# Performance work log

Hardware: AMD Instinct MI355X
Metric: run time of the kernel (lower is better)

The kernel has to match this reference:

```python
import jax, jax.numpy as jnp
import numpy as np

NV, NE, NT = 20000, 40000, 30000
D, H, L = 512, 8, 2
HD = D // H
SCALE = float(np.sqrt(HD))
EV, EE, ET = 160000, 160000, 120000
LN_EPS = 1e-5


def _layer_norm(x, g, b):
    m = jnp.mean(x, axis=-1, keepdims=True)
    v = jnp.mean((x - m) ** 2, axis=-1, keepdims=True)
    return (x - m) * jax.lax.rsqrt(v + LN_EPS) * g + b


def _attn_layer(x, ei, W, b, g, bt):
    # x: [N, D]; ei: [2, E]; W: [4, D, D] (q,k,v,out); b: [4, D]
    n = x.shape[0]
    resid = x
    q = (x @ W[0] + b[0]).reshape(n, H, HD)
    k = (x @ W[1] + b[1]).reshape(n, H, HD)
    v = (x @ W[2] + b[2]).reshape(n, H, HD)
    src, dst = ei[0], ei[1]
    # per-edge scores: query at target, key at source (k[edge_index[1]] gather in original)
    scores = jnp.sum(q[dst] * k[src], axis=-1) / SCALE        # [E, H]
    # NOTE: original applies softmax over dim=0, i.e. globally over the edge axis
    w = jax.nn.softmax(scores, axis=0)                         # [E, H]
    msgs = w[:, :, None] * v[src]                              # [E, H, HD]
    out = jax.ops.segment_sum(msgs, dst, num_segments=n)      # [N, H, HD]
    out = out.reshape(n, D) @ W[3] + b[3]
    return _layer_norm(out + resid, g, bt)


def _attn_stack(x, ei, W, b, g, bt):
    for l in range(L):
        x = _attn_layer(x, ei, W[l], b[l], g[l], bt[l])
    return x


def setup_inputs() -> dict:
    key = jax.random.key(0)
    ks = jax.random.split(key, 16)
    inp = {}
    inp['vertices'] = jax.random.normal(ks[0], (NV, D), jnp.float32)
    inp['edge_features'] = jax.random.normal(ks[1], (NE, D), jnp.float32)
    inp['triangle_features'] = jax.random.normal(ks[2], (NT, D), jnp.float32)
    inp['v_embed'] = jax.random.normal(ks[3], (NV, D), jnp.float32)
    inp['e_embed'] = jax.random.normal(ks[4], (NE, D), jnp.float32)
    inp['t_embed'] = jax.random.normal(ks[5], (NT, D), jnp.float32)
    inp['v_pos'] = jax.random.normal(ks[6], (NV, D), jnp.float32) * 0.1
    inp['e_pos'] = jax.random.normal(ks[7], (NE, D), jnp.float32) * 0.1
    inp['t_pos'] = jax.random.normal(ks[8], (NT, D), jnp.float32) * 0.1
    for name, k2 in (('v', ks[9]), ('e', ks[10]), ('t', ks[11])):
        inp[name + 'W'] = jax.random.normal(k2, (L, 4, D, D), jnp.float32) * 0.02
        inp[name + 'B'] = jnp.zeros((L, 4, D), jnp.float32)
        inp[name + 'G'] = jnp.ones((L, D), jnp.float32)
        inp[name + 'Bt'] = jnp.zeros((L, D), jnp.float32)
    inp['head_W'] = jax.random.normal(ks[12], (3, D, D), jnp.float32) * 0.02
    inp['head_b'] = jnp.zeros((3, D), jnp.float32)
    inp['v_ei'] = jax.random.randint(ks[13], (2, EV), 0, NV, jnp.int32)
    inp['e_ei'] = jax.random.randint(ks[14], (2, EE), 0, NE, jnp.int32)
    inp['t_ei'] = jax.random.randint(ks[15], (2, ET), 0, NT, jnp.int32)
    return inp


def reference(vertices, edge_features, triangle_features, v_embed, e_embed, t_embed,
              v_pos, e_pos, t_pos, vW, vB, vG, vBt, eW, eB, eG, eBt,
              tW, tB, tG, tBt, head_W, head_b, v_ei, e_ei, t_ei):
    # embedding(arange(N)) == full table lookup; add positional params and input features
    v = v_embed + v_pos + vertices
    e = e_embed + e_pos + edge_features
    t = t_embed + t_pos + triangle_features
    v = _attn_stack(v, v_ei, vW, vB, vG, vBt)
    e = _attn_stack(e, e_ei, eW, eB, eG, eBt)
    t = _attn_stack(t, t_ei, tW, tB, tG, tBt)
    v_out = v @ head_W[0] + head_b[0]
    e_out = e @ head_W[1] + head_b[1]
    t_out = t @ head_W[2] + head_b[2]
    return (v_out, e_out, t_out)
```

## Files before the change

### kernel.cpp

```cpp
#include <hip/hip_runtime.h>


typedef __attribute__((ext_vector_type(8))) __bf16 bf16x8;
typedef __attribute__((ext_vector_type(4))) float f32x4;
typedef __attribute__((ext_vector_type(8))) unsigned short ushort8v;
typedef __attribute__((ext_vector_type(4))) unsigned short ushort4v;

__device__ __forceinline__ float b2f(unsigned short u) {
  union { unsigned u; float f; } x; x.u = (unsigned)u << 16; return x.f;
}
__device__ __forceinline__ unsigned short f2b(float f) {
  union { float f; unsigned u; } x; x.f = f;
  unsigned r = x.u + 0x7fffu + ((x.u >> 16) & 1u);
  return (unsigned short)(r >> 16);
}

__global__ __launch_bounds__(256) void init_x_kernel(
    const float4* __restrict__ a, const float4* __restrict__ b,
    const float4* __restrict__ c, float4* __restrict__ x,
    unsigned short* __restrict__ xb, long long n4)
{
  long long stride = (long long)gridDim.x * 256;
  for (long long i = (long long)blockIdx.x * 256 + threadIdx.x; i < n4; i += stride) {
    float4 av = a[i], bv = b[i], cv = c[i];
    float4 r;
    r.x = av.x + bv.x + cv.x; r.y = av.y + bv.y + cv.y;
    r.z = av.z + bv.z + cv.z; r.w = av.w + bv.w + cv.w;
    x[i] = r;
    ushort4v o; o.x = f2b(r.x); o.y = f2b(r.y); o.z = f2b(r.z); o.w = f2b(r.w);
    *(ushort4v*)(xb + i * 4) = o;
  }
}

__global__ __launch_bounds__(256) void transpose_w_kernel(
    const float* __restrict__ W, unsigned short* __restrict__ WT)
{
  __shared__ float t[32][33];
  const float* src = W + (size_t)blockIdx.z * 262144;
  unsigned short* dst = WT + (size_t)blockIdx.z * 262144;
  int bx = blockIdx.x * 32, by = blockIdx.y * 32;
  int tx = threadIdx.x, ty = threadIdx.y;
  #pragma unroll
  for (int i = 0; i < 32; i += 8)
    t[ty + i][tx] = src[(size_t)(by + ty + i) * 512 + bx + tx];
  __syncthreads();
  #pragma unroll
  for (int i = 0; i < 32; i += 8) {
    int c = bx + ty + i;
    int p = (c & ~0x3C) | ((c & 0x30) >> 2) | ((c & 0x0C) << 2);
    dst[(size_t)p * 512 + by + tx] = f2b(t[tx][ty + i]);
  }
}

__device__ __forceinline__ void stage16(const void* g, void* lds_uniform) {
  __builtin_amdgcn_global_load_lds(
      (const __attribute__((address_space(1))) void*)g,
      (__attribute__((address_space(3))) void*)lds_uniform, 16, 0, 0);
}

template<int OUT_BF16>
__global__ __launch_bounds__(256) void gemm_bt_kernel(
    const unsigned short* __restrict__ A,
    const unsigned short* __restrict__ BT,
    const float* __restrict__ bias,
    void* __restrict__ Cv,
    int M, int Ncols)
{
  constexpr int K = 512;
  __shared__ unsigned short smem[32768];

  const int nwg = gridDim.x, orig = blockIdx.x;
  const int xcd = orig & 7, lin = orig >> 3;
  const int q = nwg >> 3, r8 = nwg & 7;
  const int wgid = (xcd < r8 ? xcd * (q + 1) : r8 * (q + 1) + (xcd - r8) * q) + lin;

  const int tiles_n = Ncols >> 7;
  const int tm = wgid / tiles_n;
  const int tn = wgid - tm * tiles_n;
  const int row0 = tm << 7, col0 = tn << 7;
  const int lane = threadIdx.x & 63, wid = threadIdx.x >> 6;
  const int wm = (wid >> 1) << 6, wn = (wid & 1) << 6;

  f32x4 acc[4][4];
  #pragma unroll
  for (int i = 0; i < 4; ++i)
    #pragma unroll
    for (int j = 0; j < 4; ++j) acc[i][j] = (f32x4)0.f;

  int srow[4], scsw[4], sseg[4];
  #pragma unroll
  for (int i = 0; i < 4; ++i) {
    int seg = (i << 2) | wid;
    int idx = (seg << 6) | lane;
    int row = idx >> 3, ch = idx & 7;
    sseg[i] = seg; srow[i] = row; scsw[i] = ch ^ (row & 7);
  }

  #define STAGE(buf, kb_)                                                      \
    _Pragma("unroll")                                                          \
    for (int i = 0; i < 4; ++i) {                                              \
      int ra = row0 + srow[i]; ra = (ra < M) ? ra : (M - 1);                   \
      stage16(A + (size_t)ra * K + (kb_) + (scsw[i] << 3),                     \
              smem + (buf) * 16384 + (sseg[i] << 9));                          \
      int rb = col0 + srow[i];                                                 \
      stage16(BT + (size_t)rb * K + (kb_) + (scsw[i] << 3),                    \
              smem + (buf) * 16384 + 8192 + (sseg[i] << 9));                   \
    }

  STAGE(0, 0)
  asm volatile("s_waitcnt vmcnt(0)" ::: "memory");
  __syncthreads();

  #pragma unroll
  for (int kt = 0; kt < 8; ++kt) {
    const int cur = kt & 1;
    if (kt < 7) {
      STAGE(cur ^ 1, (kt + 1) << 6)
    }
    const unsigned short* As = smem + cur * 16384;
    const unsigned short* Bs = As + 8192;
    #pragma unroll
    for (int kk = 0; kk < 2; ++kk) {
      const int kb = (kk << 6) + ((lane >> 4) << 4);
      bf16x8 af[4], bfr[4];
      #pragma unroll
      for (int mi = 0; mi < 4; ++mi) {
        int r = wm + (mi << 4) + (lane & 15);
        af[mi] = *(const bf16x8*)((const char*)As + (r << 7) + (kb ^ ((r & 7) << 4)));
      }
      #pragma unroll
      for (int ni = 0; ni < 4; ++ni) {
        int r = wn + (ni << 4) + (lane & 15);
        bfr[ni] = *(const bf16x8*)((const char*)Bs + (r << 7) + (kb ^ ((r & 7) << 4)));
      }
      #pragma unroll
      for (int mi = 0; mi < 4; ++mi)
        #pragma unroll
        for (int ni = 0; ni < 4; ++ni)
          acc[mi][ni] = __builtin_amdgcn_mfma_f32_16x16x32_bf16(
              bfr[ni], af[mi], acc[mi][ni], 0, 0, 0);
    }
    asm volatile("s_waitcnt vmcnt(0)" ::: "memory");
    __syncthreads();
  }
  #undef STAGE

  const int mrow = lane & 15;
  const int t4 = (lane >> 4) << 4;
  float bsv[16];
  #pragma unroll
  for (int ni = 0; ni < 4; ++ni) {
    float4 bv = *(const float4*)(bias + col0 + wn + t4 + (ni << 2));
    bsv[4*ni+0] = bv.x; bsv[4*ni+1] = bv.y; bsv[4*ni+2] = bv.z; bsv[4*ni+3] = bv.w;
  }

  if (OUT_BF16) {
    unsigned short* C = (unsigned short*)Cv;
    #pragma unroll
    for (int mi = 0; mi < 4; ++mi) {
      int rowg = row0 + wm + (mi << 4) + mrow;
      if (rowg < M) {
        ushort8v o0, o1;
        #pragma unroll
        for (int r = 0; r < 4; ++r) {
          o0[r]     = f2b(acc[mi][0][r] + bsv[r]);
          o0[4 + r] = f2b(acc[mi][1][r] + bsv[4 + r]);
          o1[r]     = f2b(acc[mi][2][r] + bsv[8 + r]);
          o1[4 + r] = f2b(acc[mi][3][r] + bsv[12 + r]);
        }
        unsigned short* cp = C + (size_t)rowg * Ncols + col0 + wn + t4;
        *(ushort8v*)cp = o0;
        *(ushort8v*)(cp + 8) = o1;
      }
    }
  } else {
    float* C = (float*)Cv;
    #pragma unroll
    for (int mi = 0; mi < 4; ++mi) {
      int rowg = row0 + wm + (mi << 4) + mrow;
      if (rowg < M) {
        float* cp = C + (size_t)rowg * Ncols + col0 + wn + t4;
        #pragma unroll
        for (int ni = 0; ni < 4; ++ni) {
          float4 v;
          v.x = acc[mi][ni][0] + bsv[4*ni+0];
          v.y = acc[mi][ni][1] + bsv[4*ni+1];
          v.z = acc[mi][ni][2] + bsv[4*ni+2];
          v.w = acc[mi][ni][3] + bsv[4*ni+3];
          *(float4*)(cp + (ni << 2)) = v;
        }
      }
    }
  }
}

__global__ __launch_bounds__(256) void csr_scores_kernel(
    const unsigned short* __restrict__ qkv, const int* __restrict__ srcs,
    const int* __restrict__ rowptr, int N, float* __restrict__ sc)
{
  int wid = threadIdx.x >> 6, lane = threadIdx.x & 63;
  int n = (blockIdx.x << 2) | wid;
  if (n >= N) return;
  int beg = rowptr[n], end = rowptr[n + 1];
  if (beg == end) return;
  ushort8v qv = *(const ushort8v*)(qkv + (size_t)n * 1536 + (lane << 3));
  float qf[8];
  #pragma unroll
  for (int j = 0; j < 8; ++j) qf[j] = b2f(qv[j]);
  int i = beg;
  for (; i + 2 <= end; i += 2) {
    int s0 = srcs[i], s1 = srcs[i + 1];
    ushort8v k0 = *(const ushort8v*)(qkv + (size_t)s0 * 1536 + 512 + (lane << 3));
    ushort8v k1 = *(const ushort8v*)(qkv + (size_t)s1 * 1536 + 512 + (lane << 3));
    float p0 = 0.f, p1 = 0.f;
    #pragma unroll
    for (int j = 0; j < 8; ++j) { p0 += qf[j] * b2f(k0[j]); p1 += qf[j] * b2f(k1[j]); }
    p0 += __shfl_xor(p0, 1); p1 += __shfl_xor(p1, 1);
    p0 += __shfl_xor(p0, 2); p1 += __shfl_xor(p1, 2);
    p0 += __shfl_xor(p0, 4); p1 += __shfl_xor(p1, 4);
    if (!(lane & 7)) {
      sc[(size_t)i * 8 + (lane >> 3)] = p0 * 0.125f;
      sc[(size_t)(i + 1) * 8 + (lane >> 3)] = p1 * 0.125f;
    }
  }
  if (i < end) {
    int s0 = srcs[i];
    ushort8v k0 = *(const ushort8v*)(qkv + (size_t)s0 * 1536 + 512 + (lane << 3));
    float p0 = 0.f;
    #pragma unroll
    for (int j = 0; j < 8; ++j) p0 += qf[j] * b2f(k0[j]);
    p0 += __shfl_xor(p0, 1);
    p0 += __shfl_xor(p0, 2);
    p0 += __shfl_xor(p0, 4);
    if (!(lane & 7)) sc[(size_t)i * 8 + (lane >> 3)] = p0 * 0.125f;
  }
}

template<int OP>
__device__ __forceinline__ void reduce8_block(float (&v)[8], float* red) {
  int lane = threadIdx.x & 63, wid = threadIdx.x >> 6;
  #pragma unroll
  for (int h = 0; h < 8; ++h)
    #pragma unroll
    for (int off = 1; off < 64; off <<= 1) {
      float o = __shfl_xor(v[h], off);
      v[h] = OP ? (v[h] + o) : fmaxf(v[h], o);
    }
  if (lane == 0) {
    #pragma unroll
    for (int h = 0; h < 8; ++h) red[h * 4 + wid] = v[h];
  }
  __syncthreads();
  if (threadIdx.x == 0) {
    #pragma unroll
    for (int h = 0; h < 8; ++h) {
      float r = red[h * 4];
      #pragma unroll
      for (int w = 1; w < 4; ++w)
        r = OP ? (r + red[h * 4 + w]) : fmaxf(r, red[h * 4 + w]);
      v[h] = r;
    }
  }
}

__global__ __launch_bounds__(256) void sm_max_partial_kernel(
    const float* __restrict__ sc, int E, float* __restrict__ part)
{
  __shared__ float red[32];
  float v[8];
  #pragma unroll
  for (int h = 0; h < 8; ++h) v[h] = -1e30f;
  int stride = gridDim.x * 256;
  for (int e = blockIdx.x * 256 + threadIdx.x; e < E; e += stride) {
    #pragma unroll
    for (int h = 0; h < 8; ++h) v[h] = fmaxf(v[h], sc[(size_t)e * 8 + h]);
  }
  reduce8_block<0>(v, red);
  if (threadIdx.x == 0) {
    #pragma unroll
    for (int h = 0; h < 8; ++h) part[blockIdx.x * 8 + h] = v[h];
  }
}

__global__ __launch_bounds__(256) void sm_exp_partial_kernel(
    float* __restrict__ sc, int E, const float* __restrict__ partm,
    float* __restrict__ parts)
{
  __shared__ float red[32];
  __shared__ float gmx[8];
  float v[8];
  #pragma unroll
  for (int h = 0; h < 8; ++h) v[h] = partm[threadIdx.x * 8 + h];
  reduce8_block<0>(v, red);
  if (threadIdx.x == 0) {
    #pragma unroll
    for (int h = 0; h < 8; ++h) gmx[h] = v[h];
  }
  __syncthreads();
  float gm[8];
  #pragma unroll
  for (int h = 0; h < 8; ++h) { gm[h] = gmx[h]; v[h] = 0.f; }
  int stride = gridDim.x * 256;
  for (int e = blockIdx.x * 256 + threadIdx.x; e < E; e += stride) {
    #pragma unroll
    for (int h = 0; h < 8; ++h) {
      float w = __expf(sc[(size_t)e * 8 + h] - gm[h]);
      sc[(size_t)e * 8 + h] = w;
      v[h] += w;
    }
  }
  reduce8_block<1>(v, red);
  if (threadIdx.x == 0) {
    #pragma unroll
    for (int h = 0; h < 8; ++h) parts[blockIdx.x * 8 + h] = v[h];
  }
}

template<int OP>
__global__ __launch_bounds__(256) void sm_final_kernel(
    const float* __restrict__ part, float* __restrict__ out)
{
  __shared__ float red[32];
  float v[8];
  #pragma unroll
  for (int h = 0; h < 8; ++h) v[h] = part[threadIdx.x * 8 + h];
  reduce8_block<OP>(v, red);
  if (threadIdx.x == 0) {
    #pragma unroll
    for (int h = 0; h < 8; ++h) out[h] = OP ? (1.0f / v[h]) : v[h];
  }
}

__global__ __launch_bounds__(256) void hist_kernel(
    const int* __restrict__ ei, int E, int* __restrict__ deg)
{
  int e = blockIdx.x * 256 + threadIdx.x;
  if (e < E) atomicAdd(&deg[ei[E + e]], 1);
}

__global__ __launch_bounds__(1024) void scan_part_kernel(
    const int* __restrict__ deg, int N, int* __restrict__ rowptr,
    int* __restrict__ bsums)
{
  __shared__ int wsum[16];
  int i = blockIdx.x * 1024 + threadIdx.x;
  int lane = threadIdx.x & 63, wid = threadIdx.x >> 6;
  int sv = (i < N) ? deg[i] : 0;
  #pragma unroll
  for (int off = 1; off < 64; off <<= 1) {
    int t = __shfl_up(sv, off);
    if (lane >= off) sv += t;
  }
  if (lane == 63) wsum[wid] = sv;
  __syncthreads();
  if (threadIdx.x < 16) {
    int ws = wsum[threadIdx.x];
    #pragma unroll
    for (int off = 1; off < 16; off <<= 1) {
      int t = __shfl_up(ws, off);
      if (threadIdx.x >= off) ws += t;
    }
    wsum[threadIdx.x] = ws;
  }
  __syncthreads();
  if (wid > 0) sv += wsum[wid - 1];
  if (i < N) rowptr[i + 1] = sv;
  if (threadIdx.x == 1023) bsums[blockIdx.x] = sv;
}

__global__ __launch_bounds__(64) void scan_bsums_kernel(int* bsums, int nb)
{
  int lane = threadIdx.x;
  int v = (lane < nb) ? bsums[lane] : 0;
  #pragma unroll
  for (int off = 1; off < 64; off <<= 1) {
    int t = __shfl_up(v, off);
    if (lane >= off) v += t;
  }
  int ex = __shfl_up(v, 1);
  if (lane == 0) ex = 0;
  if (lane < nb) bsums[lane] = ex;
}

__global__ __launch_bounds__(1024) void scan_add_kernel(
    int* __restrict__ rowptr, const int* __restrict__ bsums, int N)
{
  int i = blockIdx.x * 1024 + threadIdx.x;
  if (i == 0) rowptr[0] = 0;
  if (i < N && blockIdx.x > 0) rowptr[i + 1] += bsums[blockIdx.x];
}

__global__ __launch_bounds__(256) void scatter_kernel(
    const int* __restrict__ ei, int E, const int* __restrict__ rowptr,
    int* __restrict__ cur, int* __restrict__ srcs)
{
  int e = blockIdx.x * 256 + threadIdx.x;
  if (e < E) {
    int dst = ei[E + e];
    int pos = atomicAdd(&cur[dst], 1);
    srcs[rowptr[dst] + pos] = ei[e];
  }
}

__global__ __launch_bounds__(256) void aggregate_kernel(
    const unsigned short* __restrict__ qkv, const float* __restrict__ wexp,
    const float* __restrict__ ginv, const int* __restrict__ srcs,
    const int* __restrict__ rowptr, int N, unsigned short* __restrict__ agg)
{
  int wid = threadIdx.x >> 6, lane = threadIdx.x & 63;
  int n = (blockIdx.x << 2) | wid;
  if (n >= N) return;
  int beg = rowptr[n], end = rowptr[n + 1];
  int h = lane >> 3;
  float inv = ginv[h];
  float acc[8] = {0.f,0.f,0.f,0.f,0.f,0.f,0.f,0.f};
  int i = beg;
  for (; i + 2 <= end; i += 2) {
    int s0 = srcs[i], s1 = srcs[i + 1];
    float w0 = wexp[(size_t)i * 8 + h] * inv;
    float w1 = wexp[(size_t)(i + 1) * 8 + h] * inv;
    ushort8v v0 = *(const ushort8v*)(qkv + (size_t)s0 * 1536 + 1024 + (lane << 3));
    ushort8v v1 = *(const ushort8v*)(qkv + (size_t)s1 * 1536 + 1024 + (lane << 3));
    #pragma unroll
    for (int j = 0; j < 8; ++j) acc[j] += w0 * b2f(v0[j]) + w1 * b2f(v1[j]);
  }
  if (i < end) {
    int s0 = srcs[i];
    float w0 = wexp[(size_t)i * 8 + h] * inv;
    ushort8v v0 = *(const ushort8v*)(qkv + (size_t)s0 * 1536 + 1024 + (lane << 3));
    #pragma unroll
    for (int j = 0; j < 8; ++j) acc[j] += w0 * b2f(v0[j]);
  }
  ushort8v o;
  #pragma unroll
  for (int j = 0; j < 8; ++j) o[j] = f2b(acc[j]);
  *(ushort8v*)(agg + (size_t)n * 512 + (lane << 3)) = o;
}

__global__ __launch_bounds__(256) void ln_kernel(
    const unsigned short* __restrict__ proj, const float* __restrict__ g,
    const float* __restrict__ bt, float* __restrict__ x,
    unsigned short* __restrict__ xb, int N)
{
  int wid = threadIdx.x >> 6, lane = threadIdx.x & 63;
  int n = (blockIdx.x << 2) | wid;
  if (n >= N) return;
  size_t base = (size_t)n * 512 + (lane << 3);
  ushort8v pv = *(const ushort8v*)(proj + base);
  const float4* xp = (const float4*)(x + base);
  float4 x0 = xp[0], x1 = xp[1];
  float y[8] = {b2f(pv[0]) + x0.x, b2f(pv[1]) + x0.y, b2f(pv[2]) + x0.z,
                b2f(pv[3]) + x0.w, b2f(pv[4]) + x1.x, b2f(pv[5]) + x1.y,
                b2f(pv[6]) + x1.z, b2f(pv[7]) + x1.w};
  float s = 0.f;
  #pragma unroll
  for (int j = 0; j < 8; ++j) s += y[j];
  #pragma unroll
  for (int off = 1; off < 64; off <<= 1) s += __shfl_xor(s, off);
  float mean = s * (1.f / 512.f);
  float vs = 0.f;
  #pragma unroll
  for (int j = 0; j < 8; ++j) { float d = y[j] - mean; vs += d * d; }
  #pragma unroll
  for (int off = 1; off < 64; off <<= 1) vs += __shfl_xor(vs, off);
  float rstd = rsqrtf(vs * (1.f / 512.f) + 1e-5f);
  int gi = lane << 3;
  float o[8];
  #pragma unroll
  for (int j = 0; j < 8; ++j) o[j] = (y[j] - mean) * rstd * g[gi + j] + bt[gi + j];
  float4 r0 = {o[0], o[1], o[2], o[3]}, r1 = {o[4], o[5], o[6], o[7]};
  *(float4*)(x + base) = r0;
  *(float4*)(x + base + 4) = r1;
  ushort8v ob;
  #pragma unroll
  for (int j = 0; j < 8; ++j) ob[j] = f2b(o[j]);
  *(ushort8v*)(xb + base) = ob;
}

extern "C" void kernel_launch(void* const* d_in, const int* in_sizes, int n_in,
                              void* d_out, int out_size, void* d_ws, size_t ws_size,
                              hipStream_t stream)
{
  (void)n_in; (void)out_size;
  const float* feat[3] = {(const float*)d_in[0], (const float*)d_in[1], (const float*)d_in[2]};
  const float* emb[3]  = {(const float*)d_in[3], (const float*)d_in[4], (const float*)d_in[5]};
  const float* pos[3]  = {(const float*)d_in[6], (const float*)d_in[7], (const float*)d_in[8]};
  const float* W[3]  = {(const float*)d_in[9],  (const float*)d_in[13], (const float*)d_in[17]};
  const float* Bb[3] = {(const float*)d_in[10], (const float*)d_in[14], (const float*)d_in[18]};
  const float* G[3]  = {(const float*)d_in[11], (const float*)d_in[15], (const float*)d_in[19]};
  const float* Bt[3] = {(const float*)d_in[12], (const float*)d_in[16], (const float*)d_in[20]};
  const float* headW = (const float*)d_in[21];
  const float* headB = (const float*)d_in[22];
  const int* ei[3] = {(const int*)d_in[23], (const int*)d_in[24], (const int*)d_in[25]};

  int Ns[3], Es[3];
  for (int s = 0; s < 3; ++s) { Ns[s] = in_sizes[s] / 512; Es[s] = in_sizes[23 + s] / 2; }
  int NMAX = Ns[0], EMAX = Es[0];
  for (int s = 1; s < 3; ++s) { if (Ns[s] > NMAX) NMAX = Ns[s]; if (Es[s] > EMAX) EMAX = Es[s]; }

  char* base = (char*)d_ws;
  size_t off = 0;
  auto carve = [&](size_t bytes) -> char* {
    char* r = base + off;
    off += (bytes + 255) & ~(size_t)255;
    return r;
  };
  unsigned short* WT  = (unsigned short*)carve((size_t)27 * 262144 * 2);
  float*          X   = (float*)carve((size_t)NMAX * 512 * 4);
  unsigned short* XB  = (unsigned short*)carve((size_t)NMAX * 512 * 2);
  unsigned short* QKV = (unsigned short*)carve((size_t)NMAX * 1536 * 2);
  float*          SC  = (float*)carve((size_t)EMAX * 8 * 4);
  unsigned short* AGG = (unsigned short*)carve((size_t)NMAX * 512 * 2);
  int*   ROWPTR = (int*)carve((size_t)(NMAX + 1) * 4);
  int*   DEG    = (int*)carve((size_t)NMAX * 4);
  int*   SRCS   = (int*)carve((size_t)EMAX * 4);
  int*   BSUMS  = (int*)carve(64 * 4);
  float* PARTM  = (float*)carve(256 * 8 * 4);
  float* PARTS  = (float*)carve(256 * 8 * 4);
  float* GINV   = (float*)carve(256);
  unsigned short* PROJ = QKV;
  if (off > ws_size) return;

  transpose_w_kernel<<<dim3(16,16,8), dim3(32,8), 0, stream>>>(W[0], WT);
  transpose_w_kernel<<<dim3(16,16,8), dim3(32,8), 0, stream>>>(W[1], WT + (size_t)8 * 262144);
  transpose_w_kernel<<<dim3(16,16,8), dim3(32,8), 0, stream>>>(W[2], WT + (size_t)16 * 262144);
  transpose_w_kernel<<<dim3(16,16,3), dim3(32,8), 0, stream>>>(headW, WT + (size_t)24 * 262144);

  size_t out_off = 0;
  for (int s = 0; s < 3; ++s) {
    const int N = Ns[s], E = Es[s];
    const int mt = (N + 127) >> 7;
    const int nb = (N + 1023) / 1024;

    init_x_kernel<<<2048, 256, 0, stream>>>(
        (const float4*)feat[s], (const float4*)emb[s], (const float4*)pos[s],
        (float4*)X, XB, (long long)N * 128);

    hipMemsetAsync(DEG, 0, (size_t)N * 4, stream);
    hist_kernel<<<(E + 255) / 256, 256, 0, stream>>>(ei[s], E, DEG);
    scan_part_kernel<<<nb, 1024, 0, stream>>>(DEG, N, ROWPTR, BSUMS);
    scan_bsums_kernel<<<1, 64, 0, stream>>>(BSUMS, nb);
    scan_add_kernel<<<nb, 1024, 0, stream>>>(ROWPTR, BSUMS, N);
    hipMemsetAsync(DEG, 0, (size_t)N * 4, stream);
    scatter_kernel<<<(E + 255) / 256, 256, 0, stream>>>(ei[s], E, ROWPTR, DEG, SRCS);

    for (int l = 0; l < 2; ++l) {
      const unsigned short* Wqkv = WT + (size_t)(s * 8 + l * 4) * 262144;
      const unsigned short* Wo   = WT + (size_t)(s * 8 + l * 4 + 3) * 262144;
      const float* bqkv = Bb[s] + (size_t)l * 4 * 512;
      const float* bo   = Bb[s] + (size_t)(l * 4 + 3) * 512;

      gemm_bt_kernel<1><<<dim3(mt * 12), 256, 0, stream>>>(XB, Wqkv, bqkv, QKV, N, 1536);
      csr_scores_kernel<<<(N + 3) / 4, 256, 0, stream>>>(QKV, SRCS, ROWPTR, N, SC);
      sm_max_partial_kernel<<<256, 256, 0, stream>>>(SC, E, PARTM);
      sm_exp_partial_kernel<<<256, 256, 0, stream>>>(SC, E, PARTM, PARTS);
      sm_final_kernel<1><<<1, 256, 0, stream>>>(PARTS, GINV);
      aggregate_kernel<<<(N + 3) / 4, 256, 0, stream>>>(QKV, SC, GINV, SRCS, ROWPTR, N, AGG);
      gemm_bt_kernel<1><<<dim3(mt * 4), 256, 0, stream>>>(AGG, Wo, bo, PROJ, N, 512);
      ln_kernel<<<(N + 3) / 4, 256, 0, stream>>>(PROJ, G[s] + (size_t)l * 512,
                                                 Bt[s] + (size_t)l * 512, X, XB, N);
    }

    gemm_bt_kernel<0><<<dim3(mt * 4), 256, 0, stream>>>(
        XB, WT + (size_t)(24 + s) * 262144, headB + (size_t)s * 512,
        (float*)d_out + out_off, N, 512);
    out_off += (size_t)N * 512;
  }
}
```

Measured before the change: 1.498 ms.

## Retile bf16 GEMM to 256x256 blocks with 8 waves and interleaved staging

Enlarges the GEMM block tile from 128x128 to 256x256 and doubles the block to 512 threads, each wave holding an 8x4 accumulator tile. The next k-tile's async global-to-LDS loads are split into halves and interleaved with MFMA phases, separated by barriers and with wave priority raised around the MFMAs. The aim is more data reuse per LDS byte and better overlap of loads with compute. In exchange it uses 128KB of LDS, so only one block fits per CU, and the 512-column GEMMs launch far fewer blocks, which risks underfilling the GPU. It also drops the explicit vmcnt wait before consuming staged data.

Measured after the change: 1.496 ms. About the same (-0.1%).

```diff
diff --git a/kernel.cpp b/kernel.cpp
--- a/kernel.cpp
+++ b/kernel.cpp
@@ -59,7 +59,7 @@
 }
 
 template<int OUT_BF16>
-__global__ __launch_bounds__(256) void gemm_bt_kernel(
+__global__ __launch_bounds__(512, 2) void gemm_bt_kernel(
     const unsigned short* __restrict__ A,
     const unsigned short* __restrict__ BT,
     const float* __restrict__ bias,
@@ -67,98 +67,140 @@
     int M, int Ncols)
 {
   constexpr int K = 512;
-  __shared__ unsigned short smem[32768];
+  __shared__ unsigned short smem[65536];
 
   const int nwg = gridDim.x, orig = blockIdx.x;
   const int xcd = orig & 7, lin = orig >> 3;
   const int q = nwg >> 3, r8 = nwg & 7;
   const int wgid = (xcd < r8 ? xcd * (q + 1) : r8 * (q + 1) + (xcd - r8) * q) + lin;
 
-  const int tiles_n = Ncols >> 7;
+  const int tiles_n = Ncols >> 8;
   const int tm = wgid / tiles_n;
   const int tn = wgid - tm * tiles_n;
-  const int row0 = tm << 7, col0 = tn << 7;
+  const int row0 = tm << 8, col0 = tn << 8;
   const int lane = threadIdx.x & 63, wid = threadIdx.x >> 6;
-  const int wm = (wid >> 1) << 6, wn = (wid & 1) << 6;
-
-  f32x4 acc[4][4];
-  #pragma unroll
-  for (int i = 0; i < 4; ++i)
+  const int wr = (wid >> 2) << 7;
+  const int wc = (wid & 3) << 6;
+
+  f32x4 acc[8][4];
+  #pragma unroll
+  for (int i = 0; i < 8; ++i)
     #pragma unroll
     for (int j = 0; j < 4; ++j) acc[i][j] = (f32x4)0.f;
 
   int srow[4], scsw[4], sseg[4];
   #pragma unroll
   for (int i = 0; i < 4; ++i) {
-    int seg = (i << 2) | wid;
+    int seg = (i << 3) | wid;
     int idx = (seg << 6) | lane;
     int row = idx >> 3, ch = idx & 7;
     sseg[i] = seg; srow[i] = row; scsw[i] = ch ^ (row & 7);
   }
 
-  #define STAGE(buf, kb_)                                                      \
-    _Pragma("unroll")                                                          \
-    for (int i = 0; i < 4; ++i) {                                              \
-      int ra = row0 + srow[i]; ra = (ra < M) ? ra : (M - 1);                   \
-      stage16(A + (size_t)ra * K + (kb_) + (scsw[i] << 3),                     \
-              smem + (buf) * 16384 + (sseg[i] << 9));                          \
-      int rb = col0 + srow[i];                                                 \
-      stage16(BT + (size_t)rb * K + (kb_) + (scsw[i] << 3),                    \
-              smem + (buf) * 16384 + 8192 + (sseg[i] << 9));                   \
-    }
-
-  STAGE(0, 0)
-  asm volatile("s_waitcnt vmcnt(0)" ::: "memory");
+  #define STG_PAIR(buf, kb_, i)                                               \
+    { int ra = row0 + srow[i]; ra = (ra < M) ? ra : (M - 1);                  \
+      stage16(A + (size_t)ra * K + (kb_) + (scsw[i] << 3),                    \
+              smem + (buf) * 32768 + (sseg[i] << 9));                         \
+      int rb = col0 + srow[i];                                                \
+      stage16(BT + (size_t)rb * K + (kb_) + (scsw[i] << 3),                   \
+              smem + (buf) * 32768 + 16384 + (sseg[i] << 9)); }
+
+  STG_PAIR(0, 0, 0) STG_PAIR(0, 0, 1) STG_PAIR(0, 0, 2) STG_PAIR(0, 0, 3)
   __syncthreads();
 
+  const int lm = lane & 15;
+  const int kbl = (lane >> 4) << 4;
+
   #pragma unroll
   for (int kt = 0; kt < 8; ++kt) {
-    const int cur = kt & 1;
-    if (kt < 7) {
-      STAGE(cur ^ 1, (kt + 1) << 6)
-    }
-    const unsigned short* As = smem + cur * 16384;
-    const unsigned short* Bs = As + 8192;
-    #pragma unroll
-    for (int kk = 0; kk < 2; ++kk) {
-      const int kb = (kk << 6) + ((lane >> 4) << 4);
-      bf16x8 af[4], bfr[4];
+    const int cur = kt & 1, nxt = cur ^ 1, kb1 = (kt + 1) << 6;
+    const char* Asb = (const char*)(smem + cur * 32768);
+    const char* Bsb = Asb + 32768;
+
+    auto rdA = [&](int mi, int kk) -> bf16x8 {
+      int r = wr + (mi << 4) + lm;
+      int kb = (kk << 6) + kbl;
+      return *(const bf16x8*)(Asb + (r << 7) + (kb ^ ((r & 7) << 4)));
+    };
+    auto rdB = [&](int ni, int kk) -> bf16x8 {
+      int r = wc + (ni << 4) + lm;
+      int kb = (kk << 6) + kbl;
+      return *(const bf16x8*)(Bsb + (r << 7) + (kb ^ ((r & 7) << 4)));
+    };
+
+    bf16x8 av[4], bv[4];
+
+    #pragma unroll
+    for (int i = 0; i < 4; ++i) { av[i] = rdA(i, 0); bv[i] = rdB(i, 0); }
+    if (kt < 7) { STG_PAIR(nxt, kb1, 0) STG_PAIR(nxt, kb1, 1) }
+    __builtin_amdgcn_s_barrier();
+    __builtin_amdgcn_s_setprio(1);
+    #pragma unroll
+    for (int mi = 0; mi < 4; ++mi)
       #pragma unroll
-      for (int mi = 0; mi < 4; ++mi) {
-        int r = wm + (mi << 4) + (lane & 15);
-        af[mi] = *(const bf16x8*)((const char*)As + (r << 7) + (kb ^ ((r & 7) << 4)));
-      }
+      for (int ni = 0; ni < 4; ++ni)
+        acc[mi][ni] = __builtin_amdgcn_mfma_f32_16x16x32_bf16(
+            bv[ni], av[mi], acc[mi][ni], 0, 0, 0);
+    __builtin_amdgcn_s_setprio(0);
+    __builtin_amdgcn_s_barrier();
+
+    #pragma unroll
+    for (int i = 0; i < 4; ++i) av[i] = rdA(4 + i, 0);
+    if (kt < 7) { STG_PAIR(nxt, kb1, 2) STG_PAIR(nxt, kb1, 3) }
+    __builtin_amdgcn_s_barrier();
+    __builtin_amdgcn_s_setprio(1);
+    #pragma unroll
+    for (int mi = 0; mi < 4; ++mi)
       #pragma unroll
-      for (int ni = 0; ni < 4; ++ni) {
-        int r = wn + (ni << 4) + (lane & 15);
-        bfr[ni] = *(const bf16x8*)((const char*)Bs + (r << 7) + (kb ^ ((r & 7) << 4)));
-      }
+      for (int ni = 0; ni < 4; ++ni)
+        acc[4 + mi][ni] = __builtin_amdgcn_mfma_f32_16x16x32_bf16(
+            bv[ni], av[mi], acc[4 + mi][ni], 0, 0, 0);
+    __builtin_amdgcn_s_setprio(0);
+    __builtin_amdgcn_s_barrier();
+
+    #pragma unroll
+    for (int i = 0; i < 4; ++i) { av[i] = rdA(i, 1); bv[i] = rdB(i, 1); }
+    __builtin_amdgcn_s_barrier();
+    __builtin_amdgcn_s_setprio(1);
+    #pragma unroll
+    for (int mi = 0; mi < 4; ++mi)
       #pragma unroll
-      for (int mi = 0; mi < 4; ++mi)
-        #pragma unroll
-        for (int ni = 0; ni < 4; ++ni)
-          acc[mi][ni] = __builtin_amdgcn_mfma_f32_16x16x32_bf16(
-              bfr[ni], af[mi], acc[mi][ni], 0, 0, 0);
-    }
-    asm volatile("s_waitcnt vmcnt(0)" ::: "memory");
+      for (int ni = 0; ni < 4; ++ni)
+        acc[mi][ni] = __builtin_amdgcn_mfma_f32_16x16x32_bf16(
+            bv[ni], av[mi], acc[mi][ni], 0, 0, 0);
+    __builtin_amdgcn_s_setprio(0);
+    __builtin_amdgcn_s_barrier();
+
+    #pragma unroll
+    for (int i = 0; i < 4; ++i) av[i] = rdA(4 + i, 1);
+    __builtin_amdgcn_s_barrier();
+    __builtin_amdgcn_s_setprio(1);
+    #pragma unroll
+    for (int mi = 0; mi < 4; ++mi)
+      #pragma unroll
+      for (int ni = 0; ni < 4; ++ni)
+        acc[4 + mi][ni] = __builtin_amdgcn_mfma_f32_16x16x32_bf16(
+            bv[ni], av[mi], acc[4 + mi][ni], 0, 0, 0);
+    __builtin_amdgcn_s_setprio(0);
+
     __syncthreads();
   }
-  #undef STAGE
+  #undef STG_PAIR
 
   const int mrow = lane & 15;
   const int t4 = (lane >> 4) << 4;
   float bsv[16];
   #pragma unroll
   for (int ni = 0; ni < 4; ++ni) {
-    float4 bv = *(const float4*)(bias + col0 + wn + t4 + (ni << 2));
-    bsv[4*ni+0] = bv.x; bsv[4*ni+1] = bv.y; bsv[4*ni+2] = bv.z; bsv[4*ni+3] = bv.w;
+    float4 bvv = *(const float4*)(bias + col0 + wc + t4 + (ni << 2));
+    bsv[4*ni+0] = bvv.x; bsv[4*ni+1] = bvv.y; bsv[4*ni+2] = bvv.z; bsv[4*ni+3] = bvv.w;
   }
 
   if (OUT_BF16) {
     unsigned short* C = (unsigned short*)Cv;
     #pragma unroll
-    for (int mi = 0; mi < 4; ++mi) {
-      int rowg = row0 + wm + (mi << 4) + mrow;
+    for (int mi = 0; mi < 8; ++mi) {
+      int rowg = row0 + wr + (mi << 4) + mrow;
       if (rowg < M) {
         ushort8v o0, o1;
         #pragma unroll
@@ -168,7 +210,7 @@
           o1[r]     = f2b(acc[mi][2][r] + bsv[8 + r]);
           o1[4 + r] = f2b(acc[mi][3][r] + bsv[12 + r]);
         }
-        unsigned short* cp = C + (size_t)rowg * Ncols + col0 + wn + t4;
+        unsigned short* cp = C + (size_t)rowg * Ncols + col0 + wc + t4;
         *(ushort8v*)cp = o0;
         *(ushort8v*)(cp + 8) = o1;
       }
@@ -176,10 +218,10 @@
   } else {
     float* C = (float*)Cv;
     #pragma unroll
-    for (int mi = 0; mi < 4; ++mi) {
-      int rowg = row0 + wm + (mi << 4) + mrow;
+    for (int mi = 0; mi < 8; ++mi) {
+      int rowg = row0 + wr + (mi << 4) + mrow;
       if (rowg < M) {
-        float* cp = C + (size_t)rowg * Ncols + col0 + wn + t4;
+        float* cp = C + (size_t)rowg * Ncols + col0 + wc + t4;
         #pragma unroll
         for (int ni = 0; ni < 4; ++ni) {
           float4 v;
@@ -529,7 +571,7 @@
   size_t out_off = 0;
   for (int s = 0; s < 3; ++s) {
     const int N = Ns[s], E = Es[s];
-    const int mt = (N + 127) >> 7;
+    const int mt = (N + 255) >> 8;
     const int nb = (N + 1023) / 1024;
 
     init_x_kernel<<<2048, 256, 0, stream>>>(
@@ -550,18 +592,18 @@
       const float* bqkv = Bb[s] + (size_t)l * 4 * 512;
       const float* bo   = Bb[s] + (size_t)(l * 4 + 3) * 512;
 
-      gemm_bt_kernel<1><<<dim3(mt * 12), 256, 0, stream>>>(XB, Wqkv, bqkv, QKV, N, 1536);
+      gemm_bt_kernel<1><<<dim3(mt * 6), 512, 0, stream>>>(XB, Wqkv, bqkv, QKV, N, 1536);
       csr_scores_kernel<<<(N + 3) / 4, 256, 0, stream>>>(QKV, SRCS, ROWPTR, N, SC);
       sm_max_partial_kernel<<<256, 256, 0, stream>>>(SC, E, PARTM);
       sm_exp_partial_kernel<<<256, 256, 0, stream>>>(SC, E, PARTM, PARTS);
       sm_final_kernel<1><<<1, 256, 0, stream>>>(PARTS, GINV);
       aggregate_kernel<<<(N + 3) / 4, 256, 0, stream>>>(QKV, SC, GINV, SRCS, ROWPTR, N, AGG);
-      gemm_bt_kernel<1><<<dim3(mt * 4), 256, 0, stream>>>(AGG, Wo, bo, PROJ, N, 512);
+      gemm_bt_kernel<1><<<dim3(mt * 2), 512, 0, stream>>>(AGG, Wo, bo, PROJ, N, 512);
       ln_kernel<<<(N + 3) / 4, 256, 0, stream>>>(PROJ, G[s] + (size_t)l * 512,
                                                  Bt[s] + (size_t)l * 512, X, XB, N);
     }
 
-    gemm_bt_kernel<0><<<dim3(mt * 4), 256, 0, stream>>>(
+    gemm_bt_kernel<0><<<dim3(mt * 2), 512, 0, stream>>>(
         XB, WT + (size_t)(24 + s) * 262144, headB + (size_t)s * 512,
         (float*)d_out + out_off, N, 512);
     out_off += (size_t)N * 512;
```
